# Kernel optimization log

Measured on AMD Instinct MI355X. Metric: run time of the kernel, lower is better.

Reference implementation:

```python
import jax, jax.numpy as jnp
import numpy as np

B, H, W, D = 8, 128, 128, 256
N = 8192
NUM_FREQS = 10
MLP_W = 256
DEPTH = 4
IN_DIM = 2 + 4 * NUM_FREQS + 3 * D + 3  # 813


def setup_inputs() -> dict:
    key = jax.random.key(0)
    ks = jax.random.split(key, 12)
    feature_grid = jax.random.normal(ks[0], (B, H, W, D), jnp.float32)
    context_vector = jax.random.normal(ks[1], (B, D), jnp.float32)
    coords = jax.random.uniform(ks[2], (N, 2), jnp.float32, -1.0, 1.0)
    oracle_pixels = jax.random.uniform(ks[3], (B, N, 3), jnp.float32)

    def dense(k, i, o):
        return (jax.random.normal(k, (i, o), jnp.float32) / np.sqrt(i)).astype(jnp.float32)

    mlp0_w = dense(ks[4], IN_DIM, MLP_W)
    mlp0_b = jnp.zeros((MLP_W,), jnp.float32)
    mlp_hw = (jax.random.normal(ks[5], (DEPTH - 1, MLP_W, MLP_W), jnp.float32) / np.sqrt(MLP_W)).astype(jnp.float32)
    mlp_hb = jnp.zeros((DEPTH - 1, MLP_W), jnp.float32)
    ctx_w = dense(ks[6], D, 2 * MLP_W)  # FiLM context_proj (shared across depth)
    ctx_b = jnp.zeros((2 * MLP_W,), jnp.float32)
    out_w = dense(ks[7], MLP_W, 3) * 0.01  # original inits to zeros; small random for nontrivial grads
    out_b = jnp.zeros((3,), jnp.float32)
    return {
        "feature_grid": feature_grid, "context_vector": context_vector,
        "coords": coords, "oracle_pixels": oracle_pixels,
        "mlp0_w": mlp0_w, "mlp0_b": mlp0_b, "mlp_hw": mlp_hw, "mlp_hb": mlp_hb,
        "ctx_w": ctx_w, "ctx_b": ctx_b, "out_w": out_w, "out_b": out_b,
    }


def positional_encoding(coords):
    # coords: [N, 2] -> [N, 2 + 4*NUM_FREQS]; order per freq: sin(2), cos(2)
    freqs = (2.0 ** jnp.arange(NUM_FREQS, dtype=jnp.float32)) * jnp.pi  # [F]
    ang = coords[:, None, :] * freqs[None, :, None]  # [N, F, 2]
    sc = jnp.stack([jnp.sin(ang), jnp.cos(ang)], axis=2)  # [N, F, 2(sin/cos), 2]
    return jnp.concatenate([coords, sc.reshape(coords.shape[0], -1)], axis=-1)


def bilinear_sample(grid, coords):
    # grid: [B, Hl, Wl, C]; coords: [N, 2] in [-1, 1] (dim0 -> Hl, dim1 -> Wl)
    # Equivalent to map_coordinates(order=1, mode='reflect') for in-range coords.
    Hl, Wl = grid.shape[1], grid.shape[2]
    y = (coords[:, 0] + 1.0) * 0.5 * (Hl - 1)
    x = (coords[:, 1] + 1.0) * 0.5 * (Wl - 1)
    y0f = jnp.clip(jnp.floor(y), 0.0, Hl - 1)
    x0f = jnp.clip(jnp.floor(x), 0.0, Wl - 1)
    y0 = y0f.astype(jnp.int32)
    x0 = x0f.astype(jnp.int32)
    y1 = jnp.minimum(y0 + 1, Hl - 1)
    x1 = jnp.minimum(x0 + 1, Wl - 1)
    wy = (y - y0f)[None, :, None]  # [1, N, 1]
    wx = (x - x0f)[None, :, None]
    g00 = grid[:, y0, x0]  # [B, N, C]
    g01 = grid[:, y0, x1]
    g10 = grid[:, y1, x0]
    g11 = grid[:, y1, x1]
    top = g00 * (1.0 - wx) + g01 * wx
    bot = g10 * (1.0 - wx) + g11 * wx
    return top * (1.0 - wy) + bot * wy


def reference(feature_grid, context_vector, coords, oracle_pixels,
              mlp0_w, mlp0_b, mlp_hw, mlp_hb, ctx_w, ctx_b, out_w, out_b):
    enc = positional_encoding(coords)  # [N, 42]

    # 3-level pyramid via bilinear downsampling
    levels = [feature_grid,
              jax.image.resize(feature_grid, (B, H // 2, W // 2, D), 'bilinear'),
              jax.image.resize(feature_grid, (B, H // 4, W // 4, D), 'bilinear')]
    feats = jnp.concatenate([bilinear_sample(g, coords) for g in levels], axis=-1)  # [B, N, 3D]

    enc_t = jnp.broadcast_to(enc[None], (B, N, enc.shape[-1]))
    h = jnp.concatenate([enc_t, feats, oracle_pixels], axis=-1)  # [B, N, 813]

    # FiLM parameters (shared Dense across all depth iterations)
    ctx = context_vector @ ctx_w + ctx_b  # [B, 2*MLP_W]
    gamma = ctx[:, None, :MLP_W] + 1.0  # [B, 1, MLP_W]
    beta = ctx[:, None, MLP_W:]

    h = jax.nn.gelu(jnp.einsum('bnd,dk->bnk', h, mlp0_w) + mlp0_b)
    h = jax.nn.gelu((h * gamma + beta)) if False else h  # placeholder removed below
    # NOTE: correct order is Dense -> FiLM -> gelu; redo layer 0 properly:
    return _mlp_tail(None, None, None)  # never reached


def _mlp_tail(*a):
    raise NotImplementedError


# --- clean final reference (overrides the draft above) ---
def reference(feature_grid, context_vector, coords, oracle_pixels,
              mlp0_w, mlp0_b, mlp_hw, mlp_hb, ctx_w, ctx_b, out_w, out_b):
    enc = positional_encoding(coords)  # [N, 42]
    levels = [feature_grid,
              jax.image.resize(feature_grid, (B, H // 2, W // 2, D), 'bilinear'),
              jax.image.resize(feature_grid, (B, H // 4, W // 4, D), 'bilinear')]
    feats = jnp.concatenate([bilinear_sample(g, coords) for g in levels], axis=-1)  # [B, N, 3D]
    enc_t = jnp.broadcast_to(enc[None], (B, N, enc.shape[-1]))
    h = jnp.concatenate([enc_t, feats, oracle_pixels], axis=-1)  # [B, N, IN_DIM]

    ctx = context_vector @ ctx_w + ctx_b  # [B, 2*MLP_W]
    gamma = ctx[:, None, :MLP_W] + 1.0
    beta = ctx[:, None, MLP_W:]

    h = jax.nn.gelu((jnp.einsum('bnd,dk->bnk', h, mlp0_w) + mlp0_b) * gamma + beta)
    for i in range(DEPTH - 1):
        h = jax.nn.gelu((jnp.einsum('bnk,kj->bnj', h, mlp_hw[i]) + mlp_hb[i]) * gamma + beta)
    return jnp.tanh(jnp.einsum('bnk,ko->bno', h, out_w) + out_b)  # [B, N, 3]
```

## Files before the change

kernel.cpp:

```cpp
#include <hip/hip_runtime.h>
#include <math.h>
#include <stdint.h>

#define NBATCH 8
#define HGRID 128
#define DCH 256
#define NPTS 8192
#define INDIM 813
#define K0P 832
#define TOTROWS (NBATCH * NPTS)

typedef __attribute__((ext_vector_type(8))) short short8;
typedef __attribute__((ext_vector_type(16))) float f32x16;

__device__ __forceinline__ unsigned short bf16_rne(float f) {
  unsigned int u = __float_as_uint(f);
  u += 0x7fffu + ((u >> 16) & 1u);
  return (unsigned short)(u >> 16);
}
__device__ __forceinline__ float b2f(unsigned short h) {
  return __uint_as_float(((unsigned int)h) << 16);
}
__device__ __forceinline__ void split_bf16(float v, unsigned short& hi, unsigned short& lo) {
  hi = bf16_rne(v);
  lo = bf16_rne(v - b2f(hi));
}

__device__ __forceinline__ float gelu_f(float x) {
  float u = 0.7978845608028654f * (x + 0.044715f * x * x * x);
  float au = fabsf(u);
  float e = __expf(-2.0f * au);
  float t = 1.0f - 2.0f * e / (1.0f + e);
  t = copysignf(t, u);
  return 0.5f * x * (1.0f + t);
}

__device__ __forceinline__ void gload16(const void* g, void* l) {
  __builtin_amdgcn_global_load_lds(
      (const __attribute__((address_space(1))) unsigned int*)g,
      (__attribute__((address_space(3))) unsigned int*)l, 16, 0, 0);
}

__global__ __launch_bounds__(256) void ctx_kernel(
    const float* __restrict__ cv, const float* __restrict__ cw,
    const float* __restrict__ cb, float* __restrict__ gb) {
  int b = blockIdx.x;
  int t = threadIdx.x;
  for (int half = 0; half < 2; ++half) {
    int j = half * 256 + t;
    float acc = cb[j];
    for (int k = 0; k < DCH; ++k)
      acc = fmaf(cv[b * DCH + k], cw[k * 512 + j], acc);
    if (j < 256) acc += 1.0f;
    gb[b * 512 + j] = acc;
  }
}

__global__ __launch_bounds__(256) void wprep0_kernel(const float* __restrict__ w0,
                                                     unsigned short* __restrict__ thi,
                                                     unsigned short* __restrict__ tlo) {
  int k = blockIdx.x;
  int n = threadIdx.x;
  float v = (k < INDIM) ? w0[(size_t)k * 256 + n] : 0.0f;
  unsigned short h, l;
  split_bf16(v, h, l);
  size_t o = (size_t)n * K0P + k;
  thi[o] = h; tlo[o] = l;
}
__global__ __launch_bounds__(256) void wpreph_kernel(const float* __restrict__ hw,
                                                     unsigned short* __restrict__ thi,
                                                     unsigned short* __restrict__ tlo) {
  int ik = blockIdx.x;
  int i = ik >> 8, k = ik & 255;
  int n = threadIdx.x;
  float v = hw[(size_t)ik * 256 + n];
  unsigned short h, l;
  split_bf16(v, h, l);
  size_t o = (size_t)i * 65536 + (size_t)n * 256 + k;
  thi[o] = h; tlo[o] = l;
}

template <int SCALE>
__device__ __forceinline__ void mkw(int o, int nIn, float* w, int* ix) {
  const int TAPS = 2 * SCALE;
  float s = (float)(SCALE * o) + 0.5f * (float)(SCALE - 1);
  int j0 = SCALE * o + (SCALE - 2) / 2 - (SCALE - 1);
  float wsum = 0.f;
#pragma unroll
  for (int t = 0; t < TAPS; ++t) {
    int j = j0 + t;
    float wt = 1.0f - fabsf(s - (float)j) * (1.0f / (float)SCALE);
    bool valid = (j >= 0) && (j < nIn);
    wt = valid ? wt : 0.0f;
    ix[t] = valid ? j : 0;
    w[t] = wt;
    wsum += wt;
  }
  float inv = 1.0f / wsum;
#pragma unroll
  for (int t = 0; t < TAPS; ++t) w[t] *= inv;
}

template <int SCALE>
__global__ __launch_bounds__(256) void vpass_kernel(const float* __restrict__ g,
                                                    float* __restrict__ out) {
  const int HO = HGRID / SCALE;
  int pix = (blockIdx.x << 2) + (threadIdx.x >> 6);
  int lane = threadIdx.x & 63;
  int b = pix / (HO * HGRID);
  int rem = pix - b * (HO * HGRID);
  int oy = rem / HGRID, x = rem - (rem / HGRID) * HGRID;
  float wy[2 * SCALE]; int iy[2 * SCALE];
  mkw<SCALE>(oy, HGRID, wy, iy);
  float ax = 0.f, ay = 0.f, az = 0.f, aw = 0.f;
#pragma unroll
  for (int a = 0; a < 2 * SCALE; ++a) {
    if (wy[a] == 0.f) continue;
    const float4 v = *(const float4*)&g[((size_t)(b * HGRID + iy[a]) * HGRID + x) * DCH + lane * 4];
    ax = fmaf(wy[a], v.x, ax); ay = fmaf(wy[a], v.y, ay);
    az = fmaf(wy[a], v.z, az); aw = fmaf(wy[a], v.w, aw);
  }
  float4 r; r.x = ax; r.y = ay; r.z = az; r.w = aw;
  *(float4*)&out[(size_t)pix * DCH + lane * 4] = r;
}
template <int SCALE>
__global__ __launch_bounds__(256) void hpass_kernel(const float* __restrict__ v,
                                                    float* __restrict__ out) {
  const int HO = HGRID / SCALE, WO = HGRID / SCALE;
  int pix = (blockIdx.x << 2) + (threadIdx.x >> 6);
  int lane = threadIdx.x & 63;
  int b = pix / (HO * WO);
  int rem = pix - b * (HO * WO);
  int oy = rem / WO, ox = rem - (rem / WO) * WO;
  float wx[2 * SCALE]; int ix[2 * SCALE];
  mkw<SCALE>(ox, HGRID, wx, ix);
  float ax = 0.f, ay = 0.f, az = 0.f, aw = 0.f;
#pragma unroll
  for (int c = 0; c < 2 * SCALE; ++c) {
    if (wx[c] == 0.f) continue;
    const float4 t = *(const float4*)&v[((size_t)(b * HO + oy) * HGRID + ix[c]) * DCH + lane * 4];
    ax = fmaf(wx[c], t.x, ax); ay = fmaf(wx[c], t.y, ay);
    az = fmaf(wx[c], t.z, az); aw = fmaf(wx[c], t.w, aw);
  }
  float4 r; r.x = ax; r.y = ay; r.z = az; r.w = aw;
  *(float4*)&out[(size_t)pix * DCH + lane * 4] = r;
}

__device__ __forceinline__ void sample3(const float* __restrict__ g, int HW, int b,
                                        float cy, float cx, int lane,
                                        unsigned short* __restrict__ dhi,
                                        unsigned short* __restrict__ dlo) {
  float fm = (float)(HW - 1);
  float y = ((cy + 1.0f) * 0.5f) * fm;
  float x = ((cx + 1.0f) * 0.5f) * fm;
  float y0f = fminf(fmaxf(floorf(y), 0.0f), fm);
  float x0f = fminf(fmaxf(floorf(x), 0.0f), fm);
  int y0 = (int)y0f, x0 = (int)x0f;
  int y1 = min(y0 + 1, HW - 1), x1 = min(x0 + 1, HW - 1);
  float wy = y - y0f, wx = x - x0f;
  size_t bb = (size_t)b * HW * HW;
  const float4 v00 = *(const float4*)&g[(bb + (size_t)y0 * HW + x0) * DCH + lane * 4];
  const float4 v01 = *(const float4*)&g[(bb + (size_t)y0 * HW + x1) * DCH + lane * 4];
  const float4 v10 = *(const float4*)&g[(bb + (size_t)y1 * HW + x0) * DCH + lane * 4];
  const float4 v11 = *(const float4*)&g[(bb + (size_t)y1 * HW + x1) * DCH + lane * 4];
  float r[4];
  {
    float t0 = v00.x * (1.f - wx) + v01.x * wx, b0 = v10.x * (1.f - wx) + v11.x * wx;
    r[0] = t0 * (1.f - wy) + b0 * wy;
    float t1 = v00.y * (1.f - wx) + v01.y * wx, b1 = v10.y * (1.f - wx) + v11.y * wx;
    r[1] = t1 * (1.f - wy) + b1 * wy;
    float t2 = v00.z * (1.f - wx) + v01.z * wx, b2 = v10.z * (1.f - wx) + v11.z * wx;
    r[2] = t2 * (1.f - wy) + b2 * wy;
    float t3 = v00.w * (1.f - wx) + v01.w * wx, b3 = v10.w * (1.f - wx) + v11.w * wx;
    r[3] = t3 * (1.f - wy) + b3 * wy;
  }
  unsigned short h[4], l[4];
#pragma unroll
  for (int j = 0; j < 4; ++j) split_bf16(r[j], h[j], l[j]);
  ushort2 p;
  p.x = h[0]; p.y = h[1]; *(ushort2*)(dhi + lane * 4) = p;
  p.x = h[2]; p.y = h[3]; *(ushort2*)(dhi + lane * 4 + 2) = p;
  p.x = l[0]; p.y = l[1]; *(ushort2*)(dlo + lane * 4) = p;
  p.x = l[2]; p.y = l[3]; *(ushort2*)(dlo + lane * 4 + 2) = p;
}

__global__ __launch_bounds__(256) void assemble_kernel(
    const float* __restrict__ g0, const float* __restrict__ g1,
    const float* __restrict__ g2, const float* __restrict__ coords,
    const float* __restrict__ oracle, unsigned short* __restrict__ h0hi,
    unsigned short* __restrict__ h0lo, int row0, int nrows) {
  int lr = (blockIdx.x << 2) + (threadIdx.x >> 6);
  if (lr >= nrows) return;
  int lane = threadIdx.x & 63;
  int r = row0 + lr;
  int b = r >> 13, n = r & (NPTS - 1);
  float cy = coords[2 * n], cx = coords[2 * n + 1];
  unsigned short* rhi = h0hi + (size_t)lr * K0P;
  unsigned short* rlo = h0lo + (size_t)lr * K0P;
  if (lane < 45) {
    float val; int pos;
    if (lane < 2) { val = (lane == 0) ? cy : cx; pos = lane; }
    else if (lane < 42) {
      int q = lane - 2, f = q >> 2, m = q & 3;
      float ang = ((m & 1) ? cx : cy) * ldexpf(3.14159274101257324f, f);
      val = (m < 2) ? sinf(ang) : cosf(ang);
      pos = lane;
    } else { pos = 810 + (lane - 42); val = oracle[((size_t)b * NPTS + n) * 3 + (lane - 42)]; }
    unsigned short h, l; split_bf16(val, h, l);
    rhi[pos] = h; rlo[pos] = l;
  } else {
    int pos = INDIM + (lane - 45);
    rhi[pos] = 0; rlo[pos] = 0;
  }
  sample3(g0, 128, b, cy, cx, lane, rhi + 42, rlo + 42);
  sample3(g1, 64, b, cy, cx, lane, rhi + 42 + 256, rlo + 42 + 256);
  sample3(g2, 32, b, cy, cx, lane, rhi + 42 + 512, rlo + 42 + 512);
}

#define MFMA(a, b, c) __builtin_amdgcn_mfma_f32_32x32x16_bf16((a), (b), (c), 0, 0, 0)

__global__ __launch_bounds__(256) void gemm_mfma(
    const unsigned short* __restrict__ Ahi, const unsigned short* __restrict__ Alo, int lda,
    const unsigned short* __restrict__ Bhi, const unsigned short* __restrict__ Blo, int ldb,
    int K, const float* __restrict__ bias, const float* __restrict__ gb,
    unsigned short* __restrict__ Chi, unsigned short* __restrict__ Clo, int row0) {
  __shared__ alignas(16) unsigned short lds[4][8][4][16][8];
  const int tid = threadIdx.x;
  const int lane = tid & 63;
  const int wid = tid >> 6;
  const int wm = wid >> 1, wn = wid & 1;
  const int m0 = blockIdx.x << 7;
  const int n0 = blockIdx.y << 7;
  const int ri = lane & 15;
  const int kc = lane >> 4;
  const int rgbit = (lane >> 4) & 1;
  const int khalf = lane >> 5;

#define MKSRC(pl, baserow, pitch, jj) \
  ((pl) + (size_t)((baserow) + (wid * 2 + (jj)) * 16 + ri) * (pitch) + kc * 8)
  const unsigned short* sAh0 = MKSRC(Ahi, m0, lda, 0);
  const unsigned short* sAh1 = MKSRC(Ahi, m0, lda, 1);
  const unsigned short* sAl0 = MKSRC(Alo, m0, lda, 0);
  const unsigned short* sAl1 = MKSRC(Alo, m0, lda, 1);
  const unsigned short* sBh0 = MKSRC(Bhi, n0, ldb, 0);
  const unsigned short* sBh1 = MKSRC(Bhi, n0, ldb, 1);
  const unsigned short* sBl0 = MKSRC(Blo, n0, ldb, 0);
  const unsigned short* sBl1 = MKSRC(Blo, n0, ldb, 1);
  unsigned short* dAh0 = &lds[0][wid * 2 + 0][0][0][0];
  unsigned short* dAh1 = &lds[0][wid * 2 + 1][0][0][0];
  unsigned short* dAl0 = &lds[1][wid * 2 + 0][0][0][0];
  unsigned short* dAl1 = &lds[1][wid * 2 + 1][0][0][0];
  unsigned short* dBh0 = &lds[2][wid * 2 + 0][0][0][0];
  unsigned short* dBh1 = &lds[2][wid * 2 + 1][0][0][0];
  unsigned short* dBl0 = &lds[3][wid * 2 + 0][0][0][0];
  unsigned short* dBl1 = &lds[3][wid * 2 + 1][0][0][0];

  const unsigned short* Ah_base = &lds[0][wm * 4 + rgbit][khalf][ri][0];
  const unsigned short* Al_base = &lds[1][wm * 4 + rgbit][khalf][ri][0];
  const unsigned short* Bh_base = &lds[2][wn * 4 + rgbit][khalf][ri][0];
  const unsigned short* Bl_base = &lds[3][wn * 4 + rgbit][khalf][ri][0];

  f32x16 acc00 = {}, acc01 = {}, acc10 = {}, acc11 = {};

#pragma unroll 1
  for (int k0 = 0; k0 < K; k0 += 32) {
    gload16(sAh0, dAh0); gload16(sAh1, dAh1);
    gload16(sAl0, dAl0); gload16(sAl1, dAl1);
    gload16(sBh0, dBh0); gload16(sBh1, dBh1);
    gload16(sBl0, dBl0); gload16(sBl1, dBl1);
    sAh0 += 32; sAh1 += 32; sAl0 += 32; sAl1 += 32;
    sBh0 += 32; sBh1 += 32; sBl0 += 32; sBl1 += 32;
    __syncthreads();
#pragma unroll
    for (int t = 0; t < 2; ++t) {
      short8 ah0 = *(const short8*)(Ah_base + t * 256);
      short8 ah1 = *(const short8*)(Ah_base + 1024 + t * 256);
      short8 al0 = *(const short8*)(Al_base + t * 256);
      short8 al1 = *(const short8*)(Al_base + 1024 + t * 256);
      short8 bh0 = *(const short8*)(Bh_base + t * 256);
      short8 bh1 = *(const short8*)(Bh_base + 1024 + t * 256);
      short8 bl0 = *(const short8*)(Bl_base + t * 256);
      short8 bl1 = *(const short8*)(Bl_base + 1024 + t * 256);
      acc00 = MFMA(ah0, bh0, acc00);
      acc01 = MFMA(ah0, bh1, acc01);
      acc10 = MFMA(ah1, bh0, acc10);
      acc11 = MFMA(ah1, bh1, acc11);
      acc00 = MFMA(ah0, bl0, acc00);
      acc01 = MFMA(ah0, bl1, acc01);
      acc10 = MFMA(ah1, bl0, acc10);
      acc11 = MFMA(ah1, bl1, acc11);
      acc00 = MFMA(al0, bh0, acc00);
      acc01 = MFMA(al0, bh1, acc01);
      acc10 = MFMA(al1, bh0, acc10);
      acc11 = MFMA(al1, bh1, acc11);
    }
    __syncthreads();
  }

  const int bidx = (row0 + m0) >> 13;
  const float* gbb = gb + (bidx << 9);
  const int colbase = n0 + wn * 64 + (lane & 31);
  const int rowbase = m0 + wm * 64 + 4 * khalf;
#define EPI(accv, mi, ni)                                              \
  {                                                                    \
    int col = colbase + (ni)*32;                                       \
    float bi = bias[col], ga = gbb[col], be = gbb[256 + col];          \
    _Pragma("unroll") for (int rr = 0; rr < 16; ++rr) {                \
      int row = rowbase + (mi)*32 + (rr & 3) + ((rr >> 2) << 3);       \
      float v = (accv[rr] + bi) * ga + be;                             \
      v = gelu_f(v);                                                   \
      unsigned short h, l;                                             \
      split_bf16(v, h, l);                                             \
      size_t o = (size_t)row * 256 + col;                              \
      Chi[o] = h; Clo[o] = l;                                          \
    }                                                                  \
  }
  EPI(acc00, 0, 0)
  EPI(acc01, 0, 1)
  EPI(acc10, 1, 0)
  EPI(acc11, 1, 1)
}

__global__ __launch_bounds__(256) void out_kernel(
    const unsigned short* __restrict__ Hhi, const unsigned short* __restrict__ Hlo,
    const float* __restrict__ ow, const float* __restrict__ ob,
    float* __restrict__ out, int row0, int nrows) {
  int lr = (blockIdx.x << 2) + (threadIdx.x >> 6);
  if (lr >= nrows) return;
  int lane = threadIdx.x & 63;
  size_t base = (size_t)lr * 256 + (lane << 2);
  ushort4 hh = *(const ushort4*)&Hhi[base];
  ushort4 ll = *(const ushort4*)&Hlo[base];
  float hv[4];
  hv[0] = b2f(hh.x) + b2f(ll.x);
  hv[1] = b2f(hh.y) + b2f(ll.y);
  hv[2] = b2f(hh.z) + b2f(ll.z);
  hv[3] = b2f(hh.w) + b2f(ll.w);
  float s0 = 0.f, s1 = 0.f, s2 = 0.f;
#pragma unroll
  for (int j = 0; j < 4; ++j) {
    int k = (lane << 2) + j;
    s0 = fmaf(hv[j], ow[k * 3 + 0], s0);
    s1 = fmaf(hv[j], ow[k * 3 + 1], s1);
    s2 = fmaf(hv[j], ow[k * 3 + 2], s2);
  }
#pragma unroll
  for (int off = 32; off > 0; off >>= 1) {
    s0 += __shfl_down(s0, off);
    s1 += __shfl_down(s1, off);
    s2 += __shfl_down(s2, off);
  }
  if (lane == 0) {
    size_t r = (size_t)(row0 + lr);
    out[r * 3 + 0] = tanhf(s0 + ob[0]);
    out[r * 3 + 1] = tanhf(s1 + ob[1]);
    out[r * 3 + 2] = tanhf(s2 + ob[2]);
  }
}

extern "C" void kernel_launch(void* const* d_in, const int* in_sizes, int n_in,
                              void* d_out, int out_size, void* d_ws, size_t ws_size,
                              hipStream_t stream) {
  const float* feature_grid = (const float*)d_in[0];
  const float* context_vec = (const float*)d_in[1];
  const float* coords = (const float*)d_in[2];
  const float* oracle = (const float*)d_in[3];
  const float* mlp0_w = (const float*)d_in[4];
  const float* mlp0_b = (const float*)d_in[5];
  const float* mlp_hw = (const float*)d_in[6];
  const float* mlp_hb = (const float*)d_in[7];
  const float* ctx_w = (const float*)d_in[8];
  const float* ctx_b = (const float*)d_in[9];
  const float* out_w = (const float*)d_in[10];
  const float* out_b = (const float*)d_in[11];
  float* out = (float*)d_out;

  char* p = (char*)d_ws;
  float* gb = (float*)p;                 p += 8 * 512 * 4;
  unsigned short* w0t_hi = (unsigned short*)p; p += (size_t)256 * K0P * 2;
  unsigned short* w0t_lo = (unsigned short*)p; p += (size_t)256 * K0P * 2;
  unsigned short* wht_hi = (unsigned short*)p; p += (size_t)3 * 65536 * 2;
  unsigned short* wht_lo = (unsigned short*)p; p += (size_t)3 * 65536 * 2;
  float* lvl1 = (float*)p;               p += (size_t)8 * 64 * 64 * 256 * 4;
  float* lvl2 = (float*)p;               p += (size_t)8 * 32 * 32 * 256 * 4;
  float* vtmp = (float*)p;               p += (size_t)8 * 64 * 128 * 256 * 4;
  size_t fixed_bytes = (size_t)(p - (char*)d_ws);
  size_t per_row_bytes = (size_t)K0P * 2 * 2 + (size_t)256 * 2 * 2 * 2;
  long long cap = 0;
  if (ws_size > fixed_bytes) cap = (long long)((ws_size - fixed_bytes) / per_row_bytes);
  if (cap > TOTROWS) cap = TOTROWS;
  cap &= ~127LL;
  if (cap < 128) cap = 128;
  unsigned short* h0hi = (unsigned short*)p;
  unsigned short* h0lo = h0hi + (size_t)cap * K0P;
  unsigned short* hAhi = h0lo + (size_t)cap * K0P;
  unsigned short* hAlo = hAhi + (size_t)cap * 256;
  unsigned short* hBhi = hAlo + (size_t)cap * 256;
  unsigned short* hBlo = hBhi + (size_t)cap * 256;

  hipLaunchKernelGGL(ctx_kernel, dim3(8), dim3(256), 0, stream, context_vec, ctx_w, ctx_b, gb);
  hipLaunchKernelGGL(wprep0_kernel, dim3(K0P), dim3(256), 0, stream, mlp0_w, w0t_hi, w0t_lo);
  hipLaunchKernelGGL(wpreph_kernel, dim3(3 * 256), dim3(256), 0, stream, mlp_hw, wht_hi, wht_lo);
  hipLaunchKernelGGL((vpass_kernel<2>), dim3(8 * 64 * 128 / 4), dim3(256), 0, stream,
                     feature_grid, vtmp);
  hipLaunchKernelGGL((hpass_kernel<2>), dim3(8 * 64 * 64 / 4), dim3(256), 0, stream, vtmp, lvl1);
  hipLaunchKernelGGL((vpass_kernel<4>), dim3(8 * 32 * 128 / 4), dim3(256), 0, stream,
                     feature_grid, vtmp);
  hipLaunchKernelGGL((hpass_kernel<4>), dim3(8 * 32 * 32 / 4), dim3(256), 0, stream, vtmp, lvl2);

  int npass = (int)((TOTROWS + cap - 1) / cap);
  for (int ps = 0; ps < npass; ++ps) {
    int row0 = (int)((long long)ps * cap);
    int nrows = TOTROWS - row0;
    if (nrows > cap) nrows = (int)cap;
    int pb = (nrows + 3) >> 2;
    hipLaunchKernelGGL(assemble_kernel, dim3(pb), dim3(256), 0, stream, feature_grid,
                       lvl1, lvl2, coords, oracle, h0hi, h0lo, row0, nrows);
    dim3 ggrid(nrows >> 7, 2);
    hipLaunchKernelGGL(gemm_mfma, ggrid, dim3(256), 0, stream, h0hi, h0lo, K0P,
                       w0t_hi, w0t_lo, K0P, K0P, mlp0_b, gb, hAhi, hAlo, row0);
    hipLaunchKernelGGL(gemm_mfma, ggrid, dim3(256), 0, stream, hAhi, hAlo, 256,
                       wht_hi + 0 * 65536, wht_lo + 0 * 65536, 256, 256,
                       mlp_hb + 0, gb, hBhi, hBlo, row0);
    hipLaunchKernelGGL(gemm_mfma, ggrid, dim3(256), 0, stream, hBhi, hBlo, 256,
                       wht_hi + 1 * 65536, wht_lo + 1 * 65536, 256, 256,
                       mlp_hb + 256, gb, hAhi, hAlo, row0);
    hipLaunchKernelGGL(gemm_mfma, ggrid, dim3(256), 0, stream, hAhi, hAlo, 256,
                       wht_hi + 2 * 65536, wht_lo + 2 * 65536, 256, 256,
                       mlp_hb + 512, gb, hBhi, hBlo, row0);
    hipLaunchKernelGGL(out_kernel, dim3(pb), dim3(256), 0, stream, hBhi, hBlo,
                       out_w, out_b, out, row0, nrows);
  }
}
```

Baseline: 769.8 us.

## Switch MLP to fp16 activations with split-fp16 weights and double-buffered GEMM

Replaces the three-term bf16 hi/lo split GEMM with fp16 MFMA. Activations are stored as a single fp16 value and weights keep a hi/lo fp16 split, so each K step issues two MFMAs instead of three and loads one activation plane instead of two. The downsampled feature levels are stored as fp16, which halves their footprint and the gather traffic. The GEMM now double-buffers its LDS stages with one sync per iteration and sets a launch bound for two blocks per CU. In exchange, activation precision drops to fp16, which risks overflow or accuracy loss relative to the previous near-fp32 scheme.

```diff
diff --git a/kernel.cpp b/kernel.cpp
--- a/kernel.cpp
+++ b/kernel.cpp
@@ -10,20 +10,21 @@
 #define K0P 832
 #define TOTROWS (NBATCH * NPTS)
 
-typedef __attribute__((ext_vector_type(8))) short short8;
+typedef __attribute__((ext_vector_type(8))) _Float16 half8;
 typedef __attribute__((ext_vector_type(16))) float f32x16;
 
-__device__ __forceinline__ unsigned short bf16_rne(float f) {
-  unsigned int u = __float_as_uint(f);
-  u += 0x7fffu + ((u >> 16) & 1u);
-  return (unsigned short)(u >> 16);
-}
-__device__ __forceinline__ float b2f(unsigned short h) {
-  return __uint_as_float(((unsigned int)h) << 16);
-}
-__device__ __forceinline__ void split_bf16(float v, unsigned short& hi, unsigned short& lo) {
-  hi = bf16_rne(v);
-  lo = bf16_rne(v - b2f(hi));
+__device__ __forceinline__ unsigned short f2h(float v) {
+  _Float16 h = (_Float16)v;
+  union { _Float16 f; unsigned short u; } c; c.f = h; return c.u;
+}
+__device__ __forceinline__ float h2f(unsigned short u) {
+  union { unsigned short u; _Float16 f; } c; c.u = u; return (float)c.f;
+}
+__device__ __forceinline__ void split_f16(float v, unsigned short& hi, unsigned short& lo) {
+  _Float16 h = (_Float16)v;
+  _Float16 l = (_Float16)(v - (float)h);
+  union { _Float16 f; unsigned short u; } a, b; a.f = h; b.f = l;
+  hi = a.u; lo = b.u;
 }
 
 __device__ __forceinline__ float gelu_f(float x) {
@@ -63,7 +64,7 @@
   int n = threadIdx.x;
   float v = (k < INDIM) ? w0[(size_t)k * 256 + n] : 0.0f;
   unsigned short h, l;
-  split_bf16(v, h, l);
+  split_f16(v, h, l);
   size_t o = (size_t)n * K0P + k;
   thi[o] = h; tlo[o] = l;
 }
@@ -75,7 +76,7 @@
   int n = threadIdx.x;
   float v = hw[(size_t)ik * 256 + n];
   unsigned short h, l;
-  split_bf16(v, h, l);
+  split_f16(v, h, l);
   size_t o = (size_t)i * 65536 + (size_t)n * 256 + k;
   thi[o] = h; tlo[o] = l;
 }
@@ -125,7 +126,7 @@
 }
 template <int SCALE>
 __global__ __launch_bounds__(256) void hpass_kernel(const float* __restrict__ v,
-                                                    float* __restrict__ out) {
+                                                    unsigned short* __restrict__ out) {
   const int HO = HGRID / SCALE, WO = HGRID / SCALE;
   int pix = (blockIdx.x << 2) + (threadIdx.x >> 6);
   int lane = threadIdx.x & 63;
@@ -142,14 +143,14 @@
     ax = fmaf(wx[c], t.x, ax); ay = fmaf(wx[c], t.y, ay);
     az = fmaf(wx[c], t.z, az); aw = fmaf(wx[c], t.w, aw);
   }
-  float4 r; r.x = ax; r.y = ay; r.z = az; r.w = aw;
-  *(float4*)&out[(size_t)pix * DCH + lane * 4] = r;
-}
-
-__device__ __forceinline__ void sample3(const float* __restrict__ g, int HW, int b,
-                                        float cy, float cx, int lane,
-                                        unsigned short* __restrict__ dhi,
-                                        unsigned short* __restrict__ dlo) {
+  ushort4 r;
+  r.x = f2h(ax); r.y = f2h(ay); r.z = f2h(az); r.w = f2h(aw);
+  *(ushort4*)&out[(size_t)pix * DCH + lane * 4] = r;
+}
+
+__device__ __forceinline__ void sample3_f32(const float* __restrict__ g, int HW, int b,
+                                            float cy, float cx, int lane,
+                                            unsigned short* __restrict__ dst) {
   float fm = (float)(HW - 1);
   float y = ((cy + 1.0f) * 0.5f) * fm;
   float x = ((cx + 1.0f) * 0.5f) * fm;
@@ -164,39 +165,52 @@
   const float4 v10 = *(const float4*)&g[(bb + (size_t)y1 * HW + x0) * DCH + lane * 4];
   const float4 v11 = *(const float4*)&g[(bb + (size_t)y1 * HW + x1) * DCH + lane * 4];
   float r[4];
-  {
-    float t0 = v00.x * (1.f - wx) + v01.x * wx, b0 = v10.x * (1.f - wx) + v11.x * wx;
-    r[0] = t0 * (1.f - wy) + b0 * wy;
-    float t1 = v00.y * (1.f - wx) + v01.y * wx, b1 = v10.y * (1.f - wx) + v11.y * wx;
-    r[1] = t1 * (1.f - wy) + b1 * wy;
-    float t2 = v00.z * (1.f - wx) + v01.z * wx, b2 = v10.z * (1.f - wx) + v11.z * wx;
-    r[2] = t2 * (1.f - wy) + b2 * wy;
-    float t3 = v00.w * (1.f - wx) + v01.w * wx, b3 = v10.w * (1.f - wx) + v11.w * wx;
-    r[3] = t3 * (1.f - wy) + b3 * wy;
-  }
-  unsigned short h[4], l[4];
-#pragma unroll
-  for (int j = 0; j < 4; ++j) split_bf16(r[j], h[j], l[j]);
+  r[0] = (v00.x*(1.f-wx)+v01.x*wx)*(1.f-wy) + (v10.x*(1.f-wx)+v11.x*wx)*wy;
+  r[1] = (v00.y*(1.f-wx)+v01.y*wx)*(1.f-wy) + (v10.y*(1.f-wx)+v11.y*wx)*wy;
+  r[2] = (v00.z*(1.f-wx)+v01.z*wx)*(1.f-wy) + (v10.z*(1.f-wx)+v11.z*wx)*wy;
+  r[3] = (v00.w*(1.f-wx)+v01.w*wx)*(1.f-wy) + (v10.w*(1.f-wx)+v11.w*wx)*wy;
   ushort2 p;
-  p.x = h[0]; p.y = h[1]; *(ushort2*)(dhi + lane * 4) = p;
-  p.x = h[2]; p.y = h[3]; *(ushort2*)(dhi + lane * 4 + 2) = p;
-  p.x = l[0]; p.y = l[1]; *(ushort2*)(dlo + lane * 4) = p;
-  p.x = l[2]; p.y = l[3]; *(ushort2*)(dlo + lane * 4 + 2) = p;
+  p.x = f2h(r[0]); p.y = f2h(r[1]); *(ushort2*)(dst + lane * 4) = p;
+  p.x = f2h(r[2]); p.y = f2h(r[3]); *(ushort2*)(dst + lane * 4 + 2) = p;
+}
+__device__ __forceinline__ void sample3_f16(const unsigned short* __restrict__ g, int HW, int b,
+                                            float cy, float cx, int lane,
+                                            unsigned short* __restrict__ dst) {
+  float fm = (float)(HW - 1);
+  float y = ((cy + 1.0f) * 0.5f) * fm;
+  float x = ((cx + 1.0f) * 0.5f) * fm;
+  float y0f = fminf(fmaxf(floorf(y), 0.0f), fm);
+  float x0f = fminf(fmaxf(floorf(x), 0.0f), fm);
+  int y0 = (int)y0f, x0 = (int)x0f;
+  int y1 = min(y0 + 1, HW - 1), x1 = min(x0 + 1, HW - 1);
+  float wy = y - y0f, wx = x - x0f;
+  size_t bb = (size_t)b * HW * HW;
+  const ushort4 u00 = *(const ushort4*)&g[(bb + (size_t)y0 * HW + x0) * DCH + lane * 4];
+  const ushort4 u01 = *(const ushort4*)&g[(bb + (size_t)y0 * HW + x1) * DCH + lane * 4];
+  const ushort4 u10 = *(const ushort4*)&g[(bb + (size_t)y1 * HW + x0) * DCH + lane * 4];
+  const ushort4 u11 = *(const ushort4*)&g[(bb + (size_t)y1 * HW + x1) * DCH + lane * 4];
+  float r[4];
+  r[0] = (h2f(u00.x)*(1.f-wx)+h2f(u01.x)*wx)*(1.f-wy) + (h2f(u10.x)*(1.f-wx)+h2f(u11.x)*wx)*wy;
+  r[1] = (h2f(u00.y)*(1.f-wx)+h2f(u01.y)*wx)*(1.f-wy) + (h2f(u10.y)*(1.f-wx)+h2f(u11.y)*wx)*wy;
+  r[2] = (h2f(u00.z)*(1.f-wx)+h2f(u01.z)*wx)*(1.f-wy) + (h2f(u10.z)*(1.f-wx)+h2f(u11.z)*wx)*wy;
+  r[3] = (h2f(u00.w)*(1.f-wx)+h2f(u01.w)*wx)*(1.f-wy) + (h2f(u10.w)*(1.f-wx)+h2f(u11.w)*wx)*wy;
+  ushort2 p;
+  p.x = f2h(r[0]); p.y = f2h(r[1]); *(ushort2*)(dst + lane * 4) = p;
+  p.x = f2h(r[2]); p.y = f2h(r[3]); *(ushort2*)(dst + lane * 4 + 2) = p;
 }
 
 __global__ __launch_bounds__(256) void assemble_kernel(
-    const float* __restrict__ g0, const float* __restrict__ g1,
-    const float* __restrict__ g2, const float* __restrict__ coords,
-    const float* __restrict__ oracle, unsigned short* __restrict__ h0hi,
-    unsigned short* __restrict__ h0lo, int row0, int nrows) {
+    const float* __restrict__ g0, const unsigned short* __restrict__ g1,
+    const unsigned short* __restrict__ g2, const float* __restrict__ coords,
+    const float* __restrict__ oracle, unsigned short* __restrict__ h0,
+    int row0, int nrows) {
   int lr = (blockIdx.x << 2) + (threadIdx.x >> 6);
   if (lr >= nrows) return;
   int lane = threadIdx.x & 63;
   int r = row0 + lr;
   int b = r >> 13, n = r & (NPTS - 1);
   float cy = coords[2 * n], cx = coords[2 * n + 1];
-  unsigned short* rhi = h0hi + (size_t)lr * K0P;
-  unsigned short* rlo = h0lo + (size_t)lr * K0P;
+  unsigned short* row = h0 + (size_t)lr * K0P;
   if (lane < 45) {
     float val; int pos;
     if (lane < 2) { val = (lane == 0) ? cy : cx; pos = lane; }
@@ -206,136 +220,119 @@
       val = (m < 2) ? sinf(ang) : cosf(ang);
       pos = lane;
     } else { pos = 810 + (lane - 42); val = oracle[((size_t)b * NPTS + n) * 3 + (lane - 42)]; }
-    unsigned short h, l; split_bf16(val, h, l);
-    rhi[pos] = h; rlo[pos] = l;
+    row[pos] = f2h(val);
   } else {
-    int pos = INDIM + (lane - 45);
-    rhi[pos] = 0; rlo[pos] = 0;
-  }
-  sample3(g0, 128, b, cy, cx, lane, rhi + 42, rlo + 42);
-  sample3(g1, 64, b, cy, cx, lane, rhi + 42 + 256, rlo + 42 + 256);
-  sample3(g2, 32, b, cy, cx, lane, rhi + 42 + 512, rlo + 42 + 512);
-}
-
-#define MFMA(a, b, c) __builtin_amdgcn_mfma_f32_32x32x16_bf16((a), (b), (c), 0, 0, 0)
-
-__global__ __launch_bounds__(256) void gemm_mfma(
-    const unsigned short* __restrict__ Ahi, const unsigned short* __restrict__ Alo, int lda,
-    const unsigned short* __restrict__ Bhi, const unsigned short* __restrict__ Blo, int ldb,
+    row[INDIM + (lane - 45)] = 0;
+  }
+  sample3_f32(g0, 128, b, cy, cx, lane, row + 42);
+  sample3_f16(g1, 64, b, cy, cx, lane, row + 42 + 256);
+  sample3_f16(g2, 32, b, cy, cx, lane, row + 42 + 512);
+}
+
+#define MFMA16(a, b, c) __builtin_amdgcn_mfma_f32_32x32x16_f16((a), (b), (c), 0, 0, 0)
+
+__global__ __launch_bounds__(256, 2) void gemm_f16(
+    const unsigned short* __restrict__ A, int lda,
+    const unsigned short* __restrict__ Wh, const unsigned short* __restrict__ Wl, int ldb,
     int K, const float* __restrict__ bias, const float* __restrict__ gb,
-    unsigned short* __restrict__ Chi, unsigned short* __restrict__ Clo, int row0) {
-  __shared__ alignas(16) unsigned short lds[4][8][4][16][8];
+    unsigned short* __restrict__ C, int row0) {
+  __shared__ alignas(16) unsigned short SA[2][8][4][16][8];
+  __shared__ alignas(16) unsigned short SB[2][2][8][4][16][8];
   const int tid = threadIdx.x;
   const int lane = tid & 63;
   const int wid = tid >> 6;
   const int wm = wid >> 1, wn = wid & 1;
+  const int ri = lane & 15;
+  const int kq = lane >> 4;
+  const int rb = (lane >> 4) & 1;
+  const int khalf = lane >> 5;
   const int m0 = blockIdx.x << 7;
   const int n0 = blockIdx.y << 7;
-  const int ri = lane & 15;
-  const int kc = lane >> 4;
-  const int rgbit = (lane >> 4) & 1;
-  const int khalf = lane >> 5;
-
-#define MKSRC(pl, baserow, pitch, jj) \
-  ((pl) + (size_t)((baserow) + (wid * 2 + (jj)) * 16 + ri) * (pitch) + kc * 8)
-  const unsigned short* sAh0 = MKSRC(Ahi, m0, lda, 0);
-  const unsigned short* sAh1 = MKSRC(Ahi, m0, lda, 1);
-  const unsigned short* sAl0 = MKSRC(Alo, m0, lda, 0);
-  const unsigned short* sAl1 = MKSRC(Alo, m0, lda, 1);
-  const unsigned short* sBh0 = MKSRC(Bhi, n0, ldb, 0);
-  const unsigned short* sBh1 = MKSRC(Bhi, n0, ldb, 1);
-  const unsigned short* sBl0 = MKSRC(Blo, n0, ldb, 0);
-  const unsigned short* sBl1 = MKSRC(Blo, n0, ldb, 1);
-  unsigned short* dAh0 = &lds[0][wid * 2 + 0][0][0][0];
-  unsigned short* dAh1 = &lds[0][wid * 2 + 1][0][0][0];
-  unsigned short* dAl0 = &lds[1][wid * 2 + 0][0][0][0];
-  unsigned short* dAl1 = &lds[1][wid * 2 + 1][0][0][0];
-  unsigned short* dBh0 = &lds[2][wid * 2 + 0][0][0][0];
-  unsigned short* dBh1 = &lds[2][wid * 2 + 1][0][0][0];
-  unsigned short* dBl0 = &lds[3][wid * 2 + 0][0][0][0];
-  unsigned short* dBl1 = &lds[3][wid * 2 + 1][0][0][0];
-
-  const unsigned short* Ah_base = &lds[0][wm * 4 + rgbit][khalf][ri][0];
-  const unsigned short* Al_base = &lds[1][wm * 4 + rgbit][khalf][ri][0];
-  const unsigned short* Bh_base = &lds[2][wn * 4 + rgbit][khalf][ri][0];
-  const unsigned short* Bl_base = &lds[3][wn * 4 + rgbit][khalf][ri][0];
-
-  f32x16 acc00 = {}, acc01 = {}, acc10 = {}, acc11 = {};
-
+
+  f32x16 acc[2][2];
+#pragma unroll
+  for (int mi = 0; mi < 2; ++mi)
+#pragma unroll
+    for (int ni = 0; ni < 2; ++ni)
+#pragma unroll
+      for (int i = 0; i < 16; ++i) acc[mi][ni][i] = 0.f;
+
+#define STAGE(bufi, kk)                                                          \
+  {                                                                              \
+    const unsigned short* sa_ =                                                  \
+        A + (size_t)(m0 + (wid * 2) * 16 + ri) * lda + (kk) + kq * 8;            \
+    gload16(sa_, &SA[bufi][wid * 2 + 0][0][0][0]);                               \
+    gload16(sa_ + (size_t)16 * lda, &SA[bufi][wid * 2 + 1][0][0][0]);            \
+    const unsigned short* sh_ =                                                  \
+        Wh + (size_t)(n0 + (wid * 2) * 16 + ri) * ldb + (kk) + kq * 8;           \
+    gload16(sh_, &SB[bufi][0][wid * 2 + 0][0][0][0]);                            \
+    gload16(sh_ + (size_t)16 * ldb, &SB[bufi][0][wid * 2 + 1][0][0][0]);         \
+    const unsigned short* sl_ =                                                  \
+        Wl + (size_t)(n0 + (wid * 2) * 16 + ri) * ldb + (kk) + kq * 8;           \
+    gload16(sl_, &SB[bufi][1][wid * 2 + 0][0][0][0]);                            \
+    gload16(sl_ + (size_t)16 * ldb, &SB[bufi][1][wid * 2 + 1][0][0][0]);         \
+  }
+
+  const int nt = K >> 5;
+  STAGE(0, 0)
+  __syncthreads();
 #pragma unroll 1
-  for (int k0 = 0; k0 < K; k0 += 32) {
-    gload16(sAh0, dAh0); gload16(sAh1, dAh1);
-    gload16(sAl0, dAl0); gload16(sAl1, dAl1);
-    gload16(sBh0, dBh0); gload16(sBh1, dBh1);
-    gload16(sBl0, dBl0); gload16(sBl1, dBl1);
-    sAh0 += 32; sAh1 += 32; sAl0 += 32; sAl1 += 32;
-    sBh0 += 32; sBh1 += 32; sBl0 += 32; sBl1 += 32;
-    __syncthreads();
-#pragma unroll
-    for (int t = 0; t < 2; ++t) {
-      short8 ah0 = *(const short8*)(Ah_base + t * 256);
-      short8 ah1 = *(const short8*)(Ah_base + 1024 + t * 256);
-      short8 al0 = *(const short8*)(Al_base + t * 256);
-      short8 al1 = *(const short8*)(Al_base + 1024 + t * 256);
-      short8 bh0 = *(const short8*)(Bh_base + t * 256);
-      short8 bh1 = *(const short8*)(Bh_base + 1024 + t * 256);
-      short8 bl0 = *(const short8*)(Bl_base + t * 256);
-      short8 bl1 = *(const short8*)(Bl_base + 1024 + t * 256);
-      acc00 = MFMA(ah0, bh0, acc00);
-      acc01 = MFMA(ah0, bh1, acc01);
-      acc10 = MFMA(ah1, bh0, acc10);
-      acc11 = MFMA(ah1, bh1, acc11);
-      acc00 = MFMA(ah0, bl0, acc00);
-      acc01 = MFMA(ah0, bl1, acc01);
-      acc10 = MFMA(ah1, bl0, acc10);
-      acc11 = MFMA(ah1, bl1, acc11);
-      acc00 = MFMA(al0, bh0, acc00);
-      acc01 = MFMA(al0, bh1, acc01);
-      acc10 = MFMA(al1, bh0, acc10);
-      acc11 = MFMA(al1, bh1, acc11);
-    }
+  for (int t = 0; t < nt; ++t) {
+    if (t + 1 < nt) STAGE((t + 1) & 1, (t + 1) << 5)
+    const int buf = t & 1;
+    half8 a[2][2], bh[2][2], bl[2][2];
+#pragma unroll
+    for (int mi = 0; mi < 2; ++mi)
+#pragma unroll
+      for (int tt = 0; tt < 2; ++tt)
+        a[mi][tt] = *(const half8*)&SA[buf][wm * 4 + mi * 2 + rb][tt * 2 + khalf][ri][0];
+#pragma unroll
+    for (int ni = 0; ni < 2; ++ni)
+#pragma unroll
+      for (int tt = 0; tt < 2; ++tt) {
+        bh[ni][tt] = *(const half8*)&SB[buf][0][wn * 4 + ni * 2 + rb][tt * 2 + khalf][ri][0];
+        bl[ni][tt] = *(const half8*)&SB[buf][1][wn * 4 + ni * 2 + rb][tt * 2 + khalf][ri][0];
+      }
+#pragma unroll
+    for (int tt = 0; tt < 2; ++tt)
+#pragma unroll
+      for (int mi = 0; mi < 2; ++mi)
+#pragma unroll
+        for (int ni = 0; ni < 2; ++ni) {
+          acc[mi][ni] = MFMA16(a[mi][tt], bh[ni][tt], acc[mi][ni]);
+          acc[mi][ni] = MFMA16(a[mi][tt], bl[ni][tt], acc[mi][ni]);
+        }
     __syncthreads();
   }
 
   const int bidx = (row0 + m0) >> 13;
   const float* gbb = gb + (bidx << 9);
-  const int colbase = n0 + wn * 64 + (lane & 31);
-  const int rowbase = m0 + wm * 64 + 4 * khalf;
-#define EPI(accv, mi, ni)                                              \
-  {                                                                    \
-    int col = colbase + (ni)*32;                                       \
-    float bi = bias[col], ga = gbb[col], be = gbb[256 + col];          \
-    _Pragma("unroll") for (int rr = 0; rr < 16; ++rr) {                \
-      int row = rowbase + (mi)*32 + (rr & 3) + ((rr >> 2) << 3);       \
-      float v = (accv[rr] + bi) * ga + be;                             \
-      v = gelu_f(v);                                                   \
-      unsigned short h, l;                                             \
-      split_bf16(v, h, l);                                             \
-      size_t o = (size_t)row * 256 + col;                              \
-      Chi[o] = h; Clo[o] = l;                                          \
-    }                                                                  \
-  }
-  EPI(acc00, 0, 0)
-  EPI(acc01, 0, 1)
-  EPI(acc10, 1, 0)
-  EPI(acc11, 1, 1)
+#pragma unroll
+  for (int ni = 0; ni < 2; ++ni) {
+    const int col = n0 + wn * 64 + ni * 32 + (lane & 31);
+    const float bi = bias[col], ga = gbb[col], be = gbb[256 + col];
+#pragma unroll
+    for (int mi = 0; mi < 2; ++mi) {
+      const f32x16 av = acc[mi][ni];
+#pragma unroll
+      for (int r = 0; r < 16; ++r) {
+        const int row = m0 + wm * 64 + mi * 32 + (r & 3) + ((r >> 2) << 3) + 4 * khalf;
+        float v = gelu_f((av[r] + bi) * ga + be);
+        C[(size_t)row * 256 + col] = f2h(v);
+      }
+    }
+  }
+#undef STAGE
 }
 
 __global__ __launch_bounds__(256) void out_kernel(
-    const unsigned short* __restrict__ Hhi, const unsigned short* __restrict__ Hlo,
-    const float* __restrict__ ow, const float* __restrict__ ob,
-    float* __restrict__ out, int row0, int nrows) {
+    const unsigned short* __restrict__ Hf, const float* __restrict__ ow,
+    const float* __restrict__ ob, float* __restrict__ out, int row0, int nrows) {
   int lr = (blockIdx.x << 2) + (threadIdx.x >> 6);
   if (lr >= nrows) return;
   int lane = threadIdx.x & 63;
-  size_t base = (size_t)lr * 256 + (lane << 2);
-  ushort4 hh = *(const ushort4*)&Hhi[base];
-  ushort4 ll = *(const ushort4*)&Hlo[base];
-  float hv[4];
-  hv[0] = b2f(hh.x) + b2f(ll.x);
-  hv[1] = b2f(hh.y) + b2f(ll.y);
-  hv[2] = b2f(hh.z) + b2f(ll.z);
-  hv[3] = b2f(hh.w) + b2f(ll.w);
+  ushort4 h = *(const ushort4*)&Hf[(size_t)lr * 256 + (lane << 2)];
+  float hv[4] = {h2f(h.x), h2f(h.y), h2f(h.z), h2f(h.w)};
   float s0 = 0.f, s1 = 0.f, s2 = 0.f;
 #pragma unroll
   for (int j = 0; j < 4; ++j) {
@@ -381,22 +378,19 @@
   unsigned short* w0t_lo = (unsigned short*)p; p += (size_t)256 * K0P * 2;
   unsigned short* wht_hi = (unsigned short*)p; p += (size_t)3 * 65536 * 2;
   unsigned short* wht_lo = (unsigned short*)p; p += (size_t)3 * 65536 * 2;
-  float* lvl1 = (float*)p;               p += (size_t)8 * 64 * 64 * 256 * 4;
-  float* lvl2 = (float*)p;               p += (size_t)8 * 32 * 32 * 256 * 4;
+  unsigned short* lvl1 = (unsigned short*)p;   p += (size_t)8 * 64 * 64 * 256 * 2;
+  unsigned short* lvl2 = (unsigned short*)p;   p += (size_t)8 * 32 * 32 * 256 * 2;
   float* vtmp = (float*)p;               p += (size_t)8 * 64 * 128 * 256 * 4;
   size_t fixed_bytes = (size_t)(p - (char*)d_ws);
-  size_t per_row_bytes = (size_t)K0P * 2 * 2 + (size_t)256 * 2 * 2 * 2;
+  size_t per_row_bytes = (size_t)(K0P + 256 + 256) * 2;
   long long cap = 0;
   if (ws_size > fixed_bytes) cap = (long long)((ws_size - fixed_bytes) / per_row_bytes);
   if (cap > TOTROWS) cap = TOTROWS;
   cap &= ~127LL;
   if (cap < 128) cap = 128;
-  unsigned short* h0hi = (unsigned short*)p;
-  unsigned short* h0lo = h0hi + (size_t)cap * K0P;
-  unsigned short* hAhi = h0lo + (size_t)cap * K0P;
-  unsigned short* hAlo = hAhi + (size_t)cap * 256;
-  unsigned short* hBhi = hAlo + (size_t)cap * 256;
-  unsigned short* hBlo = hBhi + (size_t)cap * 256;
+  unsigned short* h0 = (unsigned short*)p;
+  unsigned short* hA = h0 + (size_t)cap * K0P;
+  unsigned short* hB = hA + (size_t)cap * 256;
 
   hipLaunchKernelGGL(ctx_kernel, dim3(8), dim3(256), 0, stream, context_vec, ctx_w, ctx_b, gb);
   hipLaunchKernelGGL(wprep0_kernel, dim3(K0P), dim3(256), 0, stream, mlp0_w, w0t_hi, w0t_lo);
@@ -415,20 +409,20 @@
     if (nrows > cap) nrows = (int)cap;
     int pb = (nrows + 3) >> 2;
     hipLaunchKernelGGL(assemble_kernel, dim3(pb), dim3(256), 0, stream, feature_grid,
-                       lvl1, lvl2, coords, oracle, h0hi, h0lo, row0, nrows);
-    dim3 ggrid(nrows >> 7, 2);
-    hipLaunchKernelGGL(gemm_mfma, ggrid, dim3(256), 0, stream, h0hi, h0lo, K0P,
-                       w0t_hi, w0t_lo, K0P, K0P, mlp0_b, gb, hAhi, hAlo, row0);
-    hipLaunchKernelGGL(gemm_mfma, ggrid, dim3(256), 0, stream, hAhi, hAlo, 256,
+                       lvl1, lvl2, coords, oracle, h0, row0, nrows);
+    dim3 ggrid((nrows + 127) >> 7, 2);
+    hipLaunchKernelGGL(gemm_f16, ggrid, dim3(256), 0, stream, h0, K0P,
+                       w0t_hi, w0t_lo, K0P, K0P, mlp0_b, gb, hA, row0);
+    hipLaunchKernelGGL(gemm_f16, ggrid, dim3(256), 0, stream, hA, 256,
                        wht_hi + 0 * 65536, wht_lo + 0 * 65536, 256, 256,
-                       mlp_hb + 0, gb, hBhi, hBlo, row0);
-    hipLaunchKernelGGL(gemm_mfma, ggrid, dim3(256), 0, stream, hBhi, hBlo, 256,
+                       mlp_hb + 0, gb, hB, row0);
+    hipLaunchKernelGGL(gemm_f16, ggrid, dim3(256), 0, stream, hB, 256,
                        wht_hi + 1 * 65536, wht_lo + 1 * 65536, 256, 256,
-                       mlp_hb + 256, gb, hAhi, hAlo, row0);
-    hipLaunchKernelGGL(gemm_mfma, ggrid, dim3(256), 0, stream, hAhi, hAlo, 256,
+                       mlp_hb + 256, gb, hA, row0);
+    hipLaunchKernelGGL(gemm_f16, ggrid, dim3(256), 0, stream, hA, 256,
                        wht_hi + 2 * 65536, wht_lo + 2 * 65536, 256, 256,
-                       mlp_hb + 512, gb, hBhi, hBlo, row0);
-    hipLaunchKernelGGL(out_kernel, dim3(pb), dim3(256), 0, stream, hBhi, hBlo,
-                       out_w, out_b, out, row0, nrows);
-  }
-}
+                       mlp_hb + 512, gb, hB, row0);
+    hipLaunchKernelGGL(out_kernel, dim3(pb), dim3(256), 0, stream, hB, out_w, out_b,
+                       out, row0, nrows);
+  }
+}
```

After: 619.4 us. -19.5%, faster.
